# Performance work log

Measured on AMD Instinct MI355X. Metric: run time of the kernel, lower is better.

## Reference

```python
import jax, jax.numpy as jnp
import numpy as np

N = 16384
DIMS = [3, 256, 256, 256, 256, 256, 256, 3]
NU = 1.0 / 100.0  # 1 / Reynold


def setup_inputs() -> dict:
    key = jax.random.key(0)
    ks = jax.random.split(key, 3 + 2 * (len(DIMS) - 1))
    inp = {
        "t": jax.random.uniform(ks[0], (N, 1), dtype=jnp.float32),
        "x": jax.random.uniform(ks[1], (N, 1), dtype=jnp.float32),
        "y": jax.random.uniform(ks[2], (N, 1), dtype=jnp.float32),
    }
    for i in range(len(DIMS) - 1):
        fan_in, fan_out = DIMS[i], DIMS[i + 1]
        # glorot_normal scale
        scale = jnp.sqrt(2.0 / (fan_in + fan_out)).astype(jnp.float32)
        inp[f"W{i}"] = jax.random.normal(ks[3 + 2 * i], (fan_in, fan_out), dtype=jnp.float32) * scale
        inp[f"b{i}"] = jax.random.normal(ks[4 + 2 * i], (fan_out,), dtype=jnp.float32) * 0.01
    return inp


def _mlp(p, params):
    # p: [3] single (t,x,y) point -> [3] (u,v,p)
    h = p
    for W, b in params[:-1]:
        h = jnp.sin(h @ W + b)
    W, b = params[-1]
    return h @ W + b


def reference(t, x, y, W0, b0, W1, b1, W2, b2, W3, b3, W4, b4, W5, b5, W6, b6):
    params = [(W0, b0), (W1, b1), (W2, b2), (W3, b3), (W4, b4), (W5, b5), (W6, b6)]
    f = lambda p: _mlp(p, params)
    txy = jnp.concatenate([t, x, y], axis=1)  # [N, 3]

    uvp = jax.vmap(f)(txy)                          # [N, 3]
    J = jax.vmap(jax.jacfwd(f))(txy)                # [N, 3(out), 3(in)]
    H = jax.vmap(jax.jacfwd(jax.jacfwd(f)))(txy)    # [N, 3(out), 3(in), 3(in)]

    u, v = uvp[:, 0], uvp[:, 1]
    u_t, u_x, u_y = J[:, 0, 0], J[:, 0, 1], J[:, 0, 2]
    v_t, v_x, v_y = J[:, 1, 0], J[:, 1, 1], J[:, 1, 2]
    p_x, p_y = J[:, 2, 1], J[:, 2, 2]
    u_xx, u_yy = H[:, 0, 1, 1], H[:, 0, 2, 2]
    v_xx, v_yy = H[:, 1, 1, 1], H[:, 1, 2, 2]

    eq1 = u_t + (u * u_x + v * u_y) + p_x - NU * (u_xx + u_yy)
    eq2 = v_t + (u * v_x + v * v_y) + p_y - NU * (v_xx + v_yy)
    eq3 = u_x + v_y
    return eq1[:, None], eq2[:, None], eq3[:, None]
```

## Files before the change

kernel.cpp:

```cpp
#include <hip/hip_runtime.h>

#define NPTS 16384
#define PW 16
#define NU (1.0f / 100.0f)

typedef _Float16 f16;
typedef __attribute__((ext_vector_type(8))) _Float16 f16x8;
typedef __attribute__((ext_vector_type(4))) float f32x4;

__device__ __forceinline__ int swz(int g) { return g ^ ((g >> 3) & 7); }

__global__ __launch_bounds__(256) void prep_kernel(
    const float* __restrict__ W1, const float* __restrict__ W2,
    const float* __restrict__ W3, const float* __restrict__ W4,
    const float* __restrict__ W5, const float* __restrict__ W6,
    f16* __restrict__ bh, f16* __restrict__ b6h)
{
    int idx = blockIdx.x * 256 + threadIdx.x;
    if (idx < 40960) {
        int col = idx & 255, subk = (idx >> 8) & 3, kc = (idx >> 10) & 7, L = idx >> 13;
        const float* W = (L == 0) ? W1 : (L == 1) ? W2 : (L == 2) ? W3 : (L == 3) ? W4 : W5;
        f16x8 vh;
        #pragma unroll
        for (int j = 0; j < 8; ++j) {
            int k = kc * 32 + subk * 8 + j;
            vh[j] = (f16)W[k * 256 + col];
        }
        int nf = col >> 4, l15 = col & 15, lane = subk * 16 + l15;
        *(f16x8*)(bh + (((L * 8 + kc) * 16 + nf) * 64 + lane) * 8) = vh;
    } else {
        int u = idx - 40960;
        if (u < 512) {
            int col = u & 15, subk = (u >> 4) & 3, kc = u >> 6;
            f16x8 vh;
            #pragma unroll
            for (int j = 0; j < 8; ++j) {
                int k = kc * 32 + subk * 8 + j;
                vh[j] = (f16)((col < 3) ? W6[k * 3 + col] : 0.f);
            }
            *(f16x8*)(b6h + (kc * 64 + subk * 16 + col) * 8) = vh;
        }
    }
}

__global__ __launch_bounds__(256) void pinn_ns_mfma(
    const float* __restrict__ t_, const float* __restrict__ x_, const float* __restrict__ y_,
    const float* __restrict__ W0, const float* __restrict__ b0,
    const float* __restrict__ b1, const float* __restrict__ b2,
    const float* __restrict__ b3, const float* __restrict__ b4,
    const float* __restrict__ b5, const float* __restrict__ b6,
    const f16* __restrict__ bh, const f16* __restrict__ b6h,
    float* __restrict__ out)
{
    __shared__ __align__(16) f16 afrag[6 * 8 * 512];
    __shared__ float z6buf[6 * 16 * 4];

    const int tid = threadIdx.x;
    const int lane = tid & 63;
    const int nq = tid >> 6;
    const int gl = swz(lane);
    const int p0 = blockIdx.x * PW;

    {
        int j = tid;
        float wt = W0[j], wx = W0[256 + j], wy = W0[512 + j], bb0 = b0[j];
        int kc = j >> 5, sub = (j >> 3) & 3, jj = j & 7;
        #pragma unroll
        for (int p = 0; p < PW; ++p) {
            float tv = t_[p0 + p], xv = x_[p0 + p], yv = y_[p0 + p];
            float z = tv * wt + xv * wx + yv * wy + bb0;
            float sv, cv;
            __sincosf(z, &sv, &cv);
            float nv[6] = {sv, cv * wt, cv * wx, cv * wy, -sv * wx * wx, -sv * wy * wy};
            int g = swz(sub * 16 + p);
            #pragma unroll
            for (int c = 0; c < 6; ++c)
                afrag[((c * 8 + kc) * 64 + g) * 8 + jj] = (f16)nv[c];
        }
    }
    __syncthreads();

    const float* bias[5] = {b1, b2, b3, b4, b5};
    const f16x8* A = (const f16x8*)afrag;
    for (int L = 0; L < 5; ++L) {
        const f16x8* bH = (const f16x8*)bh + L * 8192;
        f32x4 acc[6][4];
        #pragma unroll
        for (int c = 0; c < 6; ++c)
            #pragma unroll
            for (int f = 0; f < 4; ++f)
                acc[c][f] = (f32x4){0.f, 0.f, 0.f, 0.f};

        f16x8 Bc[4];
        #pragma unroll
        for (int f = 0; f < 4; ++f)
            Bc[f] = bH[(nq * 4 + f) * 64 + lane];

        #pragma unroll
        for (int kc = 0; kc < 8; ++kc) {
            f16x8 Bn[4];
            if (kc < 7) {
                #pragma unroll
                for (int f = 0; f < 4; ++f)
                    Bn[f] = bH[((kc + 1) * 16 + nq * 4 + f) * 64 + lane];
            }
            #pragma unroll
            for (int c = 0; c < 6; ++c) {
                f16x8 Ah = A[(c * 8 + kc) * 64 + gl];
                #pragma unroll
                for (int f = 0; f < 4; ++f)
                    acc[c][f] = __builtin_amdgcn_mfma_f32_16x16x32_f16(Ah, Bc[f], acc[c][f], 0, 0, 0);
            }
            if (kc < 7) {
                #pragma unroll
                for (int f = 0; f < 4; ++f)
                    Bc[f] = Bn[f];
            }
        }
        __syncthreads();

        const float* bbp = bias[L];
        #pragma unroll
        for (int f = 0; f < 4; ++f) {
            int col = nq * 64 + f * 16 + (lane & 15);
            int kcw = col >> 5;
            int sub = (col >> 3) & 3, jj = col & 7;
            float bvf = bbp[col];
            #pragma unroll
            for (int r = 0; r < 4; ++r) {
                int rw = (lane >> 4) * 4 + r;
                float z = acc[0][f][r] + bvf;
                float zt = acc[1][f][r], zx = acc[2][f][r], zy = acc[3][f][r];
                float zxx = acc[4][f][r], zyy = acc[5][f][r];
                float sv, cv;
                __sincosf(z, &sv, &cv);
                float nv[6] = {sv, cv * zt, cv * zx, cv * zy,
                               cv * zxx - sv * zx * zx, cv * zyy - sv * zy * zy};
                int g = swz(sub * 16 + rw);
                #pragma unroll
                for (int c = 0; c < 6; ++c)
                    afrag[((c * 8 + kcw) * 64 + g) * 8 + jj] = (f16)nv[c];
            }
        }
        __syncthreads();
    }

    for (int cc = nq; cc < 6; cc += 4) {
        f32x4 a6 = {0.f, 0.f, 0.f, 0.f};
        const f16x8* b6H = (const f16x8*)b6h;
        #pragma unroll
        for (int kc = 0; kc < 8; ++kc) {
            f16x8 Ah = A[(cc * 8 + kc) * 64 + gl];
            a6 = __builtin_amdgcn_mfma_f32_16x16x32_f16(Ah, b6H[kc * 64 + lane], a6, 0, 0, 0);
        }
        int col = lane & 15;
        if (col < 3) {
            float badd = (cc == 0) ? b6[col] : 0.f;
            #pragma unroll
            for (int r = 0; r < 4; ++r)
                z6buf[(cc * 16 + (lane >> 4) * 4 + r) * 4 + col] = a6[r] + badd;
        }
    }
    __syncthreads();

    if (tid < PW) {
        int p = tid, g = p0 + p;
        float u_  = z6buf[(0  + p) * 4 + 0], v_  = z6buf[(0  + p) * 4 + 1];
        float ut  = z6buf[(16 + p) * 4 + 0], vt  = z6buf[(16 + p) * 4 + 1];
        float ux  = z6buf[(32 + p) * 4 + 0], vx  = z6buf[(32 + p) * 4 + 1], px = z6buf[(32 + p) * 4 + 2];
        float uy  = z6buf[(48 + p) * 4 + 0], vy  = z6buf[(48 + p) * 4 + 1], py = z6buf[(48 + p) * 4 + 2];
        float uxx = z6buf[(64 + p) * 4 + 0], vxx = z6buf[(64 + p) * 4 + 1];
        float uyy = z6buf[(80 + p) * 4 + 0], vyy = z6buf[(80 + p) * 4 + 1];
        out[g]            = ut + (u_ * ux + v_ * uy) + px - NU * (uxx + uyy);
        out[NPTS + g]     = vt + (u_ * vx + v_ * vy) + py - NU * (vxx + vyy);
        out[2 * NPTS + g] = ux + vy;
    }
}

extern "C" void kernel_launch(void* const* d_in, const int* in_sizes, int n_in,
                              void* d_out, int out_size, void* d_ws, size_t ws_size,
                              hipStream_t stream) {
    const float* t_ = (const float*)d_in[0];
    const float* x_ = (const float*)d_in[1];
    const float* y_ = (const float*)d_in[2];
    const float* W[7];
    const float* b[7];
    for (int i = 0; i < 7; ++i) {
        W[i] = (const float*)d_in[3 + 2 * i];
        b[i] = (const float*)d_in[4 + 2 * i];
    }
    float* out = (float*)d_out;

    f16* bh  = (f16*)d_ws;
    f16* b6h = bh + 5 * 65536;

    hipLaunchKernelGGL(prep_kernel, dim3(162), dim3(256), 0, stream,
                       W[1], W[2], W[3], W[4], W[5], W[6], bh, b6h);
    hipLaunchKernelGGL(pinn_ns_mfma, dim3(NPTS / PW), dim3(256), 0, stream,
                       t_, x_, y_, W[0], b[0],
                       b[1], b[2], b[3], b[4], b[5], b[6],
                       bh, b6h, out);
}
```

Before: 151.6 us.

## Swap MFMA operand roles so activations write back as packed f16x4 stores

Swaps the A/B operands of the MFMA so weights become the row operand and activations the column operand. Each lane's accumulator now holds four consecutive features of one point, so the sin/cos epilogue writes packed f16x4 vectors to LDS instead of scalar f16 stores. The first layer is reorganized the same way with vectorized W0/b0 loads. The final layer runs in one wavefront with six accumulators and computes the residuals straight from registers, dropping the z6buf shared buffer and its barrier. This cuts LDS store instructions and a sync, but leaves three wavefronts idle in the last layer.

Result: faster. 146.6 us (-3.3%).

```diff
diff --git a/kernel.cpp b/kernel.cpp
--- a/kernel.cpp
+++ b/kernel.cpp
@@ -5,6 +5,7 @@
 #define NU (1.0f / 100.0f)
 
 typedef _Float16 f16;
+typedef __attribute__((ext_vector_type(4))) _Float16 f16x4;
 typedef __attribute__((ext_vector_type(8))) _Float16 f16x8;
 typedef __attribute__((ext_vector_type(4))) float f32x4;
 
@@ -53,29 +54,45 @@
     float* __restrict__ out)
 {
     __shared__ __align__(16) f16 afrag[6 * 8 * 512];
-    __shared__ float z6buf[6 * 16 * 4];
 
     const int tid = threadIdx.x;
     const int lane = tid & 63;
     const int nq = tid >> 6;
+    const int q = lane >> 4;
+    const int s = lane & 15;
     const int gl = swz(lane);
     const int p0 = blockIdx.x * PW;
 
     {
-        int j = tid;
-        float wt = W0[j], wx = W0[256 + j], wy = W0[512 + j], bb0 = b0[j];
-        int kc = j >> 5, sub = (j >> 3) & 3, jj = j & 7;
-        #pragma unroll
-        for (int p = 0; p < PW; ++p) {
-            float tv = t_[p0 + p], xv = x_[p0 + p], yv = y_[p0 + p];
-            float z = tv * wt + xv * wx + yv * wy + bb0;
-            float sv, cv;
-            __sincosf(z, &sv, &cv);
-            float nv[6] = {sv, cv * wt, cv * wx, cv * wy, -sv * wx * wx, -sv * wy * wy};
-            int g = swz(sub * 16 + p);
-            #pragma unroll
-            for (int c = 0; c < 6; ++c)
-                afrag[((c * 8 + kc) * 64 + g) * 8 + jj] = (f16)nv[c];
+        float tv = t_[p0 + s], xv = x_[p0 + s], yv = y_[p0 + s];
+        int fq0 = tid >> 4;
+        #pragma unroll
+        for (int i = 0; i < 4; ++i) {
+            int fq = fq0 + 16 * i;
+            int f0 = fq * 4;
+            f32x4 w0 = *(const f32x4*)&W0[f0];
+            f32x4 w1 = *(const f32x4*)&W0[256 + f0];
+            f32x4 w2 = *(const f32x4*)&W0[512 + f0];
+            f32x4 bb = *(const f32x4*)&b0[f0];
+            f16x4 o[6];
+            #pragma unroll
+            for (int ff = 0; ff < 4; ++ff) {
+                float z = tv * w0[ff] + xv * w1[ff] + yv * w2[ff] + bb[ff];
+                float sv, cv;
+                __sincosf(z, &sv, &cv);
+                o[0][ff] = (f16)sv;
+                o[1][ff] = (f16)(cv * w0[ff]);
+                o[2][ff] = (f16)(cv * w1[ff]);
+                o[3][ff] = (f16)(cv * w2[ff]);
+                o[4][ff] = (f16)(-sv * w1[ff] * w1[ff]);
+                o[5][ff] = (f16)(-sv * w2[ff] * w2[ff]);
+            }
+            int kc = fq >> 3;
+            int g = swz(16 * ((fq >> 1) & 3) + s);
+            int half = fq & 1;
+            #pragma unroll
+            for (int c = 0; c < 6; ++c)
+                *(f16x4*)&afrag[(c * 8 + kc) * 512 + g * 8 + half * 4] = o[c];
         }
     }
     __syncthreads();
@@ -83,7 +100,7 @@
     const float* bias[5] = {b1, b2, b3, b4, b5};
     const f16x8* A = (const f16x8*)afrag;
     for (int L = 0; L < 5; ++L) {
-        const f16x8* bH = (const f16x8*)bh + L * 8192;
+        const f16x8* wH = (const f16x8*)bh + L * 8192;
         f32x4 acc[6][4];
         #pragma unroll
         for (int c = 0; c < 6; ++c)
@@ -91,89 +108,91 @@
             for (int f = 0; f < 4; ++f)
                 acc[c][f] = (f32x4){0.f, 0.f, 0.f, 0.f};
 
-        f16x8 Bc[4];
+        f16x8 Wc[4];
         #pragma unroll
         for (int f = 0; f < 4; ++f)
-            Bc[f] = bH[(nq * 4 + f) * 64 + lane];
+            Wc[f] = wH[(nq * 4 + f) * 64 + lane];
 
         #pragma unroll
         for (int kc = 0; kc < 8; ++kc) {
-            f16x8 Bn[4];
+            f16x8 Wn[4];
             if (kc < 7) {
                 #pragma unroll
                 for (int f = 0; f < 4; ++f)
-                    Bn[f] = bH[((kc + 1) * 16 + nq * 4 + f) * 64 + lane];
-            }
-            #pragma unroll
-            for (int c = 0; c < 6; ++c) {
-                f16x8 Ah = A[(c * 8 + kc) * 64 + gl];
+                    Wn[f] = wH[((kc + 1) * 16 + nq * 4 + f) * 64 + lane];
+            }
+            f16x8 S[6];
+            #pragma unroll
+            for (int c = 0; c < 6; ++c)
+                S[c] = A[(c * 8 + kc) * 64 + gl];
+            #pragma unroll
+            for (int c = 0; c < 6; ++c)
                 #pragma unroll
                 for (int f = 0; f < 4; ++f)
-                    acc[c][f] = __builtin_amdgcn_mfma_f32_16x16x32_f16(Ah, Bc[f], acc[c][f], 0, 0, 0);
-            }
+                    acc[c][f] = __builtin_amdgcn_mfma_f32_16x16x32_f16(Wc[f], S[c], acc[c][f], 0, 0, 0);
             if (kc < 7) {
                 #pragma unroll
                 for (int f = 0; f < 4; ++f)
-                    Bc[f] = Bn[f];
+                    Wc[f] = Wn[f];
             }
         }
         __syncthreads();
 
         const float* bbp = bias[L];
         #pragma unroll
-        for (int f = 0; f < 4; ++f) {
-            int col = nq * 64 + f * 16 + (lane & 15);
-            int kcw = col >> 5;
-            int sub = (col >> 3) & 3, jj = col & 7;
-            float bvf = bbp[col];
+        for (int mf = 0; mf < 4; ++mf) {
+            int fbase = nq * 64 + mf * 16 + 4 * q;
+            f32x4 bq = *(const f32x4*)&bbp[fbase];
+            f16x4 o[6];
             #pragma unroll
             for (int r = 0; r < 4; ++r) {
-                int rw = (lane >> 4) * 4 + r;
-                float z = acc[0][f][r] + bvf;
-                float zt = acc[1][f][r], zx = acc[2][f][r], zy = acc[3][f][r];
-                float zxx = acc[4][f][r], zyy = acc[5][f][r];
+                float z = acc[0][mf][r] + bq[r];
+                float zt = acc[1][mf][r], zx = acc[2][mf][r], zy = acc[3][mf][r];
+                float zxx = acc[4][mf][r], zyy = acc[5][mf][r];
                 float sv, cv;
                 __sincosf(z, &sv, &cv);
-                float nv[6] = {sv, cv * zt, cv * zx, cv * zy,
-                               cv * zxx - sv * zx * zx, cv * zyy - sv * zy * zy};
-                int g = swz(sub * 16 + rw);
-                #pragma unroll
-                for (int c = 0; c < 6; ++c)
-                    afrag[((c * 8 + kcw) * 64 + g) * 8 + jj] = (f16)nv[c];
-            }
+                o[0][r] = (f16)sv;
+                o[1][r] = (f16)(cv * zt);
+                o[2][r] = (f16)(cv * zx);
+                o[3][r] = (f16)(cv * zy);
+                o[4][r] = (f16)(cv * zxx - sv * zx * zx);
+                o[5][r] = (f16)(cv * zyy - sv * zy * zy);
+            }
+            int kc = 2 * nq + (mf >> 1);
+            int g = swz(16 * (2 * (mf & 1) + (q >> 1)) + s);
+            int half = q & 1;
+            #pragma unroll
+            for (int c = 0; c < 6; ++c)
+                *(f16x4*)&afrag[(c * 8 + kc) * 512 + g * 8 + half * 4] = o[c];
         }
         __syncthreads();
     }
 
-    for (int cc = nq; cc < 6; cc += 4) {
-        f32x4 a6 = {0.f, 0.f, 0.f, 0.f};
-        const f16x8* b6H = (const f16x8*)b6h;
+    if (nq == 0) {
+        f32x4 a6[6];
+        #pragma unroll
+        for (int c = 0; c < 6; ++c)
+            a6[c] = (f32x4){0.f, 0.f, 0.f, 0.f};
+        const f16x8* w6 = (const f16x8*)b6h;
         #pragma unroll
         for (int kc = 0; kc < 8; ++kc) {
-            f16x8 Ah = A[(cc * 8 + kc) * 64 + gl];
-            a6 = __builtin_amdgcn_mfma_f32_16x16x32_f16(Ah, b6H[kc * 64 + lane], a6, 0, 0, 0);
-        }
-        int col = lane & 15;
-        if (col < 3) {
-            float badd = (cc == 0) ? b6[col] : 0.f;
-            #pragma unroll
-            for (int r = 0; r < 4; ++r)
-                z6buf[(cc * 16 + (lane >> 4) * 4 + r) * 4 + col] = a6[r] + badd;
-        }
-    }
-    __syncthreads();
-
-    if (tid < PW) {
-        int p = tid, g = p0 + p;
-        float u_  = z6buf[(0  + p) * 4 + 0], v_  = z6buf[(0  + p) * 4 + 1];
-        float ut  = z6buf[(16 + p) * 4 + 0], vt  = z6buf[(16 + p) * 4 + 1];
-        float ux  = z6buf[(32 + p) * 4 + 0], vx  = z6buf[(32 + p) * 4 + 1], px = z6buf[(32 + p) * 4 + 2];
-        float uy  = z6buf[(48 + p) * 4 + 0], vy  = z6buf[(48 + p) * 4 + 1], py = z6buf[(48 + p) * 4 + 2];
-        float uxx = z6buf[(64 + p) * 4 + 0], vxx = z6buf[(64 + p) * 4 + 1];
-        float uyy = z6buf[(80 + p) * 4 + 0], vyy = z6buf[(80 + p) * 4 + 1];
-        out[g]            = ut + (u_ * ux + v_ * uy) + px - NU * (uxx + uyy);
-        out[NPTS + g]     = vt + (u_ * vx + v_ * vy) + py - NU * (vxx + vyy);
-        out[2 * NPTS + g] = ux + vy;
+            f16x8 Wf = w6[kc * 64 + lane];
+            #pragma unroll
+            for (int c = 0; c < 6; ++c)
+                a6[c] = __builtin_amdgcn_mfma_f32_16x16x32_f16(Wf, A[(c * 8 + kc) * 64 + gl], a6[c], 0, 0, 0);
+        }
+        if (lane < 16) {
+            int g = p0 + s;
+            float u_  = a6[0][0] + b6[0], v_ = a6[0][1] + b6[1];
+            float ut  = a6[1][0], vt  = a6[1][1];
+            float ux  = a6[2][0], vx  = a6[2][1], px = a6[2][2];
+            float uy  = a6[3][0], vy  = a6[3][1], py = a6[3][2];
+            float uxx = a6[4][0], vxx = a6[4][1];
+            float uyy = a6[5][0], vyy = a6[5][1];
+            out[g]            = ut + (u_ * ux + v_ * uy) + px - NU * (uxx + uyy);
+            out[NPTS + g]     = vt + (u_ * vx + v_ * vy) + py - NU * (vxx + vyy);
+            out[2 * NPTS + g] = ux + vy;
+        }
     }
 }
 
```
